# Optimization experiments

Hardware: AMD Instinct MI355X
Metric: run time of the kernel (lower is better)

## Reference

```python
import jax, jax.numpy as jnp
import numpy as np

B, T, SD = 16, 512, 64          # batch, action seq len, sample_dim
EMB, HD = 1024, 64              # emb_dim, head_dim
NH = EMB // HD                  # 16 heads
DEPTH, NREG, LAT, FF = 8, 16, 256, 4 * EMB
S = T + NREG                    # total sequence length (actions + registers)


def setup_inputs() -> dict:
    key = jax.random.key(0)
    ks = jax.random.split(key, 16)
    def n(k, shape, scale=0.02):
        return jax.random.normal(k, shape, jnp.float32) * scale
    return {
        "sample": jax.random.normal(ks[0], (B, T, SD), jnp.float32),
        "W_emb": n(ks[1], (SD, EMB)), "b_emb": jnp.zeros((EMB,), jnp.float32),
        "pos": n(ks[2], (T, EMB)),
        "registers": n(ks[3], (NREG, EMB), 1.0),
        "ln1_s": jnp.ones((DEPTH, EMB), jnp.float32), "ln1_b": jnp.zeros((DEPTH, EMB), jnp.float32),
        "W_qkv": n(ks[4], (DEPTH, EMB, 3 * EMB)), "b_qkv": jnp.zeros((DEPTH, 3 * EMB), jnp.float32),
        "W_o": n(ks[5], (DEPTH, EMB, EMB)), "b_o": jnp.zeros((DEPTH, EMB), jnp.float32),
        "ln2_s": jnp.ones((DEPTH, EMB), jnp.float32), "ln2_b": jnp.zeros((DEPTH, EMB), jnp.float32),
        "W_fc1": n(ks[6], (DEPTH, EMB, FF)), "b_fc1": jnp.zeros((DEPTH, FF), jnp.float32),
        "W_fc2": n(ks[7], (DEPTH, FF, EMB)), "b_fc2": jnp.zeros((DEPTH, EMB), jnp.float32),
        "lnf_s": jnp.ones((EMB,), jnp.float32), "lnf_b": jnp.zeros((EMB,), jnp.float32),
        "W_head": n(ks[8], (EMB, LAT)), "b_head": jnp.zeros((LAT,), jnp.float32),
    }


def _ln(x, s, b):
    m = jnp.mean(x, -1, keepdims=True)
    v = jnp.var(x, -1, keepdims=True)
    return (x - m) * jax.lax.rsqrt(v + 1e-5) * s + b


def _causal_last_mask():
    # True = attended to. Actions attend to all actions but NOT registers;
    # registers attend to all actions and causally (incl. self) to registers.
    allowed = jnp.ones((S, S), jnp.bool_)
    allowed = allowed.at[:T, T:].set(False)
    allowed = allowed.at[T:, T:].set(jnp.tril(jnp.ones((NREG, NREG), jnp.bool_)))
    return allowed


def reference(sample, W_emb, b_emb, pos, registers, ln1_s, ln1_b, W_qkv, b_qkv,
              W_o, b_o, ln2_s, ln2_b, W_fc1, b_fc1, W_fc2, b_fc2,
              lnf_s, lnf_b, W_head, b_head):
    # embed + positional add
    x = sample @ W_emb + b_emb + pos[None, :, :]          # [B,T,E]
    # concat registers
    x = jnp.concatenate([x, jnp.broadcast_to(registers, (B, NREG, EMB))], axis=1)  # [B,S,E]
    mask = _causal_last_mask()                             # [S,S]
    scale = 1.0 / jnp.sqrt(jnp.asarray(HD, x.dtype))
    for i in range(DEPTH):
        # pre-LN multi-head attention with structured block mask
        h = _ln(x, ln1_s[i], ln1_b[i])
        qkv = h @ W_qkv[i] + b_qkv[i]
        q, k, v = jnp.split(qkv, 3, axis=-1)
        q = q.reshape(B, S, NH, HD)
        k = k.reshape(B, S, NH, HD)
        v = v.reshape(B, S, NH, HD)
        att = jnp.einsum('bqhd,bkhd->bhqk', q, k) * scale
        att = jnp.where(mask[None, None], att, jnp.finfo(att.dtype).min)
        att = jax.nn.softmax(att, axis=-1)
        o = jnp.einsum('bhqk,bkhd->bqhd', att, v).reshape(B, S, EMB)
        x = x + o @ W_o[i] + b_o[i]
        # pre-LN MLP
        h2 = _ln(x, ln2_s[i], ln2_b[i])
        x = x + jax.nn.gelu(h2 @ W_fc1[i] + b_fc1[i]) @ W_fc2[i] + b_fc2[i]
    x = _ln(x, lnf_s, lnf_b)
    # head applied to register positions only
    return x[:, T:] @ W_head + b_head                      # [B,NREG,LAT]
```

## Files before the change

kernel.cpp:

```cpp
#include <hip/hip_runtime.h>
#include <hip/hip_bf16.h>


typedef unsigned short u16;
typedef __attribute__((ext_vector_type(4))) float f32x4;
typedef __attribute__((ext_vector_type(8))) __bf16 bf16x8;

#define DEV static __device__ __forceinline__

constexpr int Bb = 16, Tt = 512, E = 1024, HD = 64, NHd = 16;
constexpr int DEPTH = 8, NREG = 16, LAT = 256, FF = 4096;
constexpr int S = Tt + NREG;
constexpr int SPAD = 576;
constexpr int MR = Bb * S;
constexpr int ME = Bb * Tt;

DEV u16 f2bf(float f) {
  unsigned u = __builtin_bit_cast(unsigned, f);
  u += 0x7fffu + ((u >> 16) & 1u);
  return (u16)(u >> 16);
}

DEV void gll16(const u16* g, u16* l) {
  __builtin_amdgcn_global_load_lds((const __attribute__((address_space(1))) void*)g,
                                   (__attribute__((address_space(3))) void*)l, 16, 0, 0);
}

enum { M_EMBED, M_QKV, M_OPROJ, M_FC1, M_FC2, M_HEAD };

struct GA {
  const u16* A; const u16* Bt;
  int K, lda, ldb, Nrows, ldc;
  const float* bias; const float* pos;
  float* fout; u16* bout;
  u16 *qp, *kp, *vtp;
};

template<int MODE, int BN>
__global__ __launch_bounds__(256)
void gemm_bt(GA g) {
  constexpr int NI = BN / 32;
  __shared__ __align__(16) u16 As[128 * 32];
  __shared__ __align__(16) u16 Bs[BN * 32];
  const int tid = threadIdx.x;
  const u16* A  = g.A;
  const u16* Bt = g.Bt;
  const int tM = blockIdx.y, tN = blockIdx.x;

  const int lane = tid & 63, wid = tid >> 6;
  const int wr = wid >> 1, wc = wid & 1;
  const int fr = lane & 15, fg = lane >> 4;

  const int arow = tM * 128 + (tid >> 2);
  int br0 = tN * BN + (tid >> 2);
  if (br0 > g.Nrows - 1) br0 = g.Nrows - 1;
  int br1 = tN * BN + 64 + (tid >> 2);
  if (br1 > g.Nrows - 1) br1 = g.Nrows - 1;
  const int kseg = (tid & 3) * 8;
  u16* lA = As + (tid & 192) * 8;
  u16* lB = Bs + (tid & 192) * 8;

  f32x4 acc[4][NI];
#pragma unroll
  for (int i = 0; i < 4; ++i)
#pragma unroll
    for (int j = 0; j < NI; ++j) acc[i][j] = f32x4{0.f, 0.f, 0.f, 0.f};

  const int nk = g.K >> 5;
  for (int kt = 0; kt < nk; ++kt) {
    const int k0 = kt << 5;
    gll16(A + (long)arow        * g.lda + k0 + kseg, lA);
    gll16(A + (long)(arow + 64) * g.lda + k0 + kseg, lA + 2048);
    gll16(Bt + (long)br0        * g.ldb + k0 + kseg, lB);
    if (BN == 128)
      gll16(Bt + (long)br1      * g.ldb + k0 + kseg, lB + 2048);
    __syncthreads();
    bf16x8 af[4], bfr[NI];
#pragma unroll
    for (int mi = 0; mi < 4; ++mi)
      af[mi] = *(const bf16x8*)&As[(wr * 64 + mi * 16 + fr) * 32 + fg * 8];
#pragma unroll
    for (int ni = 0; ni < NI; ++ni)
      bfr[ni] = *(const bf16x8*)&Bs[(wc * (BN / 2) + ni * 16 + fr) * 32 + fg * 8];
#pragma unroll
    for (int mi = 0; mi < 4; ++mi)
#pragma unroll
      for (int ni = 0; ni < NI; ++ni)
        acc[mi][ni] = __builtin_amdgcn_mfma_f32_16x16x32_bf16(af[mi], bfr[ni], acc[mi][ni], 0, 0, 0);
    __syncthreads();
  }

#pragma unroll
  for (int mi = 0; mi < 4; ++mi)
#pragma unroll
    for (int ni = 0; ni < NI; ++ni)
#pragma unroll
      for (int j = 0; j < 4; ++j) {
        const int row = tM * 128 + wr * 64 + mi * 16 + fg * 4 + j;
        const int col = tN * BN + wc * (BN / 2) + ni * 16 + fr;
        float v = acc[mi][ni][j];
        if (MODE == M_EMBED) {
          const int b = row >> 9, t = row & 511;
          v += g.bias[col] + g.pos[(long)t * E + col];
          g.fout[((long)(b * S + t)) * E + col] = v;
        } else if (MODE == M_QKV) {
          const int b = row / S, s = row - b * S;
          v += g.bias[col];
          const int part = col >> 10, c = col & 1023;
          const int hh = c >> 6, d = c & 63;
          const u16 bf = f2bf(v);
          if (part == 0)      g.qp [((long)((b * NHd + hh) * SPAD + s)) * HD + d] = bf;
          else if (part == 1) g.kp [((long)((b * NHd + hh) * SPAD + s)) * HD + d] = bf;
          else                g.vtp[((long)((b * NHd + hh) * HD   + d)) * SPAD + s] = bf;
        } else if (MODE == M_OPROJ || MODE == M_FC2) {
          const long idx = (long)row * g.ldc + col;
          g.fout[idx] += v + g.bias[col];
        } else if (MODE == M_FC1) {
          v += g.bias[col];
          const float z = 0.7978845608028654f * (v + 0.044715f * v * v * v);
          const float e = __expf(2.f * z);
          const float th = 1.f - 2.f / (e + 1.f);
          g.bout[(long)row * g.ldc + col] = f2bf(0.5f * v * (1.f + th));
        } else if (MODE == M_HEAD) {
          g.fout[(long)row * g.ldc + col] = v + g.bias[col];
        }
      }
}

__global__ __launch_bounds__(256)
void flash_k(const u16* __restrict__ q, const u16* __restrict__ k,
             const u16* __restrict__ vt, u16* __restrict__ o) {
  __shared__ __align__(16) u16 Ks[64 * 64];
  __shared__ __align__(16) u16 Vs[64 * 64];
  __shared__ __align__(16) u16 Ps[4 * 16 * 64];
  const int tid = threadIdx.x;
  const int lane = tid & 63, w = tid >> 6;
  const int fr = lane & 15, fg = lane >> 4;
  const int qt = blockIdx.x, bh = blockIdx.y;
  const int q0 = qt * 64;

  const u16* qrow = q + ((long)bh * SPAD + q0 + w * 16 + fr) * HD;
  const bf16x8 qf0 = *(const bf16x8*)(qrow + fg * 8);
  const bf16x8 qf1 = *(const bf16x8*)(qrow + 32 + fg * 8);

  const int srow = lane >> 3, sseg = (lane & 7) * 8;
  const u16* kg = k  + ((long)bh * SPAD + w * 16 + srow) * HD + sseg;
  const u16* vg = vt + ((long)(bh * HD + w * 16 + srow)) * SPAD + sseg;
  u16* lk = Ks + w * 16 * HD;
  u16* lv = Vs + w * 16 * HD;

  float m[4], lsum[4]; f32x4 oa[4];
#pragma unroll
  for (int j = 0; j < 4; ++j) { m[j] = -1e30f; lsum[j] = 0.f; }
#pragma unroll
  for (int n = 0; n < 4; ++n) oa[n] = f32x4{0.f, 0.f, 0.f, 0.f};

  const int nt = (q0 < Tt) ? 8 : 9;
  for (int kt = 0; kt < nt; ++kt) {
    __syncthreads();
    gll16(kg + kt * 64 * HD,          lk);
    gll16(kg + kt * 64 * HD + 8 * HD, lk + 8 * HD);
    gll16(vg + kt * 64,               lv);
    gll16(vg + kt * 64 + 8 * SPAD,    lv + 8 * HD);
    __syncthreads();

    f32x4 sfr[4];
#pragma unroll
    for (int n = 0; n < 4; ++n) {
      const bf16x8 kf0 = *(const bf16x8*)&Ks[(n * 16 + fr) * HD + fg * 8];
      const bf16x8 kf1 = *(const bf16x8*)&Ks[(n * 16 + fr) * HD + 32 + fg * 8];
      sfr[n] = __builtin_amdgcn_mfma_f32_16x16x32_bf16(qf0, kf0, f32x4{0.f,0.f,0.f,0.f}, 0, 0, 0);
      sfr[n] = __builtin_amdgcn_mfma_f32_16x16x32_bf16(qf1, kf1, sfr[n], 0, 0, 0);
    }
    float p[4][4];
#pragma unroll
    for (int j = 0; j < 4; ++j) {
      const int qg = q0 + w * 16 + fg * 4 + j;
      const int vlim = qg < Tt ? Tt : qg + 1;
#pragma unroll
      for (int n = 0; n < 4; ++n) {
        const int col = kt * 64 + n * 16 + fr;
        p[n][j] = (col < vlim) ? sfr[n][j] * 0.125f : -1e30f;
      }
    }
#pragma unroll
    for (int j = 0; j < 4; ++j) {
      float pm = fmaxf(fmaxf(p[0][j], p[1][j]), fmaxf(p[2][j], p[3][j]));
#pragma unroll
      for (int msk = 1; msk <= 8; msk <<= 1) pm = fmaxf(pm, __shfl_xor(pm, msk));
      const float mn = fmaxf(m[j], pm);
      const float corr = __expf(m[j] - mn);
      m[j] = mn;
      float rs = 0.f;
#pragma unroll
      for (int n = 0; n < 4; ++n) { const float e = __expf(p[n][j] - mn); p[n][j] = e; rs += e; }
#pragma unroll
      for (int msk = 1; msk <= 8; msk <<= 1) rs += __shfl_xor(rs, msk);
      lsum[j] = lsum[j] * corr + rs;
#pragma unroll
      for (int n = 0; n < 4; ++n) oa[n][j] *= corr;
    }
#pragma unroll
    for (int j = 0; j < 4; ++j)
#pragma unroll
      for (int n = 0; n < 4; ++n)
        Ps[w * 1024 + (fg * 4 + j) * 64 + n * 16 + fr] = f2bf(p[n][j]);
    __syncthreads();
    const bf16x8 pf0 = *(const bf16x8*)&Ps[w * 1024 + fr * 64 + fg * 8];
    const bf16x8 pf1 = *(const bf16x8*)&Ps[w * 1024 + fr * 64 + 32 + fg * 8];
#pragma unroll
    for (int n = 0; n < 4; ++n) {
      const bf16x8 vf0 = *(const bf16x8*)&Vs[(n * 16 + fr) * HD + fg * 8];
      const bf16x8 vf1 = *(const bf16x8*)&Vs[(n * 16 + fr) * HD + 32 + fg * 8];
      oa[n] = __builtin_amdgcn_mfma_f32_16x16x32_bf16(pf0, vf0, oa[n], 0, 0, 0);
      oa[n] = __builtin_amdgcn_mfma_f32_16x16x32_bf16(pf1, vf1, oa[n], 0, 0, 0);
    }
  }

  const int b = bh >> 4, hh = bh & 15;
#pragma unroll
  for (int j = 0; j < 4; ++j) {
    const int qg = q0 + w * 16 + fg * 4 + j;
    if (qg < S) {
      const float inv = 1.f / lsum[j];
#pragma unroll
      for (int n = 0; n < 4; ++n)
        o[((long)(b * S + qg)) * E + hh * HD + n * 16 + fr] = f2bf(oa[n][j] * inv);
    }
  }
}

__global__ __launch_bounds__(256)
void ln_k(const float* __restrict__ x, const float* __restrict__ sc,
          const float* __restrict__ bi, u16* __restrict__ out, int gather) {
  const int r = blockIdx.x;
  const int srow = gather ? ((r >> 4) * S + Tt + (r & 15)) : r;
  const float4 v = ((const float4*)(x + (long)srow * E))[threadIdx.x];
  float s = v.x + v.y + v.z + v.w;
  float q = v.x * v.x + v.y * v.y + v.z * v.z + v.w * v.w;
#pragma unroll
  for (int o = 32; o; o >>= 1) { s += __shfl_down(s, o); q += __shfl_down(q, o); }
  __shared__ float ps[8];
  if ((threadIdx.x & 63) == 0) { ps[threadIdx.x >> 6] = s; ps[4 + (threadIdx.x >> 6)] = q; }
  __syncthreads();
  s = ps[0] + ps[1] + ps[2] + ps[3];
  q = ps[4] + ps[5] + ps[6] + ps[7];
  const float mean = s * (1.f / E);
  const float rs = rsqrtf(q * (1.f / E) - mean * mean + 1e-5f);
  const int c = threadIdx.x * 4;
  ushort4 o4;
  o4.x = f2bf((v.x - mean) * rs * sc[c + 0] + bi[c + 0]);
  o4.y = f2bf((v.y - mean) * rs * sc[c + 1] + bi[c + 1]);
  o4.z = f2bf((v.z - mean) * rs * sc[c + 2] + bi[c + 2]);
  o4.w = f2bf((v.w - mean) * rs * sc[c + 3] + bi[c + 3]);
  ((ushort4*)(out + (long)r * E))[threadIdx.x] = o4;
}

__global__ __launch_bounds__(256)
void wtrans(const float* __restrict__ src, u16* __restrict__ dst, int R, int C) {
  __shared__ float t[32][33];
  const int c0 = blockIdx.x * 32, r0 = blockIdx.y * 32;
  const int tx = threadIdx.x & 31, ty = threadIdx.x >> 5;
#pragma unroll
  for (int i = 0; i < 32; i += 8) t[ty + i][tx] = src[(long)(r0 + ty + i) * C + c0 + tx];
  __syncthreads();
#pragma unroll
  for (int i = 0; i < 32; i += 8) dst[(long)(c0 + ty + i) * R + r0 + tx] = f2bf(t[tx][ty + i]);
}

__global__ void cvt_bf(const float* __restrict__ in, u16* __restrict__ out, long n) {
  const long i = ((long)blockIdx.x * blockDim.x + threadIdx.x) * 4;
  if (i >= n) return;
  const float4 v = *(const float4*)(in + i);
  ushort4 o; o.x = f2bf(v.x); o.y = f2bf(v.y); o.z = f2bf(v.z); o.w = f2bf(v.w);
  *(ushort4*)(out + i) = o;
}

__global__ void zero_k(float4* p, long n) {
  long i = (long)blockIdx.x * blockDim.x + threadIdx.x;
  const long st = (long)gridDim.x * blockDim.x;
  const float4 z = make_float4(0.f, 0.f, 0.f, 0.f);
  for (; i < n; i += st) p[i] = z;
}

__global__ void reg_copy(const float* __restrict__ regs, float* __restrict__ x) {
  const int b = blockIdx.x >> 4, r = blockIdx.x & 15;
  const float4* sp = (const float4*)(regs + (long)r * E);
  float4* dp = (float4*)(x + ((long)(b * S + Tt + r)) * E);
  dp[threadIdx.x] = sp[threadIdx.x];
}

constexpr long OFF_WQKV = 0L;
constexpr long OFF_WO   = OFF_WQKV + 3072L * 1024 * 2;
constexpr long OFF_WFC1 = OFF_WO   + 1024L * 1024 * 2;
constexpr long OFF_WFC2 = OFF_WFC1 + 4096L * 1024 * 2;
constexpr long OFF_WEMB = OFF_WFC2 + 1024L * 4096 * 2;
constexpr long OFF_WHEAD= OFF_WEMB + 1024L * 64 * 2;
constexpr long OFF_SMP  = OFF_WHEAD+ 256L * 1024 * 2;
constexpr long OFF_X    = OFF_SMP  + (long)ME * 64 * 2;
constexpr long OFF_H    = OFF_X    + (long)MR * E * 4;
constexpr long OFF_Q    = OFF_H    + (long)MR * E * 2;
constexpr long OFF_K    = OFF_Q    + 256L * SPAD * HD * 2;
constexpr long OFF_VT   = OFF_K    + 256L * SPAD * HD * 2;
constexpr long OFF_O    = OFF_VT   + 256L * SPAD * HD * 2;
constexpr long OFF_HF   = OFF_O    + (long)MR * FF * 2;
constexpr long WS_NEED  = OFF_HF   + 256L * 1024 * 2;

extern "C" void kernel_launch(void* const* d_in, const int* in_sizes, int n_in,
                              void* d_out, int out_size, void* d_ws, size_t ws_size,
                              hipStream_t stream) {
  if (ws_size < (size_t)WS_NEED) return;

  const float* sample = (const float*)d_in[0];
  const float* W_emb  = (const float*)d_in[1];
  const float* b_emb  = (const float*)d_in[2];
  const float* pos    = (const float*)d_in[3];
  const float* regs   = (const float*)d_in[4];
  const float* ln1_s  = (const float*)d_in[5];
  const float* ln1_b  = (const float*)d_in[6];
  const float* W_qkv  = (const float*)d_in[7];
  const float* b_qkv  = (const float*)d_in[8];
  const float* W_o    = (const float*)d_in[9];
  const float* b_o    = (const float*)d_in[10];
  const float* ln2_s  = (const float*)d_in[11];
  const float* ln2_b  = (const float*)d_in[12];
  const float* W_fc1  = (const float*)d_in[13];
  const float* b_fc1  = (const float*)d_in[14];
  const float* W_fc2  = (const float*)d_in[15];
  const float* b_fc2  = (const float*)d_in[16];
  const float* lnf_s  = (const float*)d_in[17];
  const float* lnf_b  = (const float*)d_in[18];
  const float* W_head = (const float*)d_in[19];
  const float* b_head = (const float*)d_in[20];

  char* w = (char*)d_ws;
  u16* wqkvT = (u16*)(w + OFF_WQKV);
  u16* woT   = (u16*)(w + OFF_WO);
  u16* wfc1T = (u16*)(w + OFF_WFC1);
  u16* wfc2T = (u16*)(w + OFF_WFC2);
  u16* wembT = (u16*)(w + OFF_WEMB);
  u16* wheadT= (u16*)(w + OFF_WHEAD);
  u16* smp   = (u16*)(w + OFF_SMP);
  float* x   = (float*)(w + OFF_X);
  u16* h     = (u16*)(w + OFF_H);
  u16* qp    = (u16*)(w + OFF_Q);
  u16* kp    = (u16*)(w + OFF_K);
  u16* vtp   = (u16*)(w + OFF_VT);
  u16* o     = (u16*)(w + OFF_O);
  u16* a1    = (u16*)(w + OFF_O);
  u16* hf    = (u16*)(w + OFF_HF);

  wtrans<<<dim3(32, 2, 1), 256, 0, stream>>>(W_emb,  wembT, 64, 1024);
  wtrans<<<dim3(8, 32, 1), 256, 0, stream>>>(W_head, wheadT, 1024, 256);
  cvt_bf<<<dim3(512), 256, 0, stream>>>(sample, smp, (long)ME * 64);
  zero_k<<<dim3(2048), 256, 0, stream>>>((float4*)qp, (3L * 256 * SPAD * HD * 2) / 16);

  {
    GA g{}; g.A = smp; g.Bt = wembT; g.K = 64; g.lda = 64; g.ldb = 64;
    g.Nrows = E; g.bias = b_emb; g.pos = pos; g.fout = x;
    gemm_bt<M_EMBED, 64><<<dim3(16, 64, 1), 256, 0, stream>>>(g);
  }
  reg_copy<<<dim3(256), 256, 0, stream>>>(regs, x);

  for (int L = 0; L < DEPTH; ++L) {
    wtrans<<<dim3(96, 32, 1),  256, 0, stream>>>(W_qkv + (long)L * 1024 * 3072, wqkvT, 1024, 3072);
    wtrans<<<dim3(32, 32, 1),  256, 0, stream>>>(W_o   + (long)L * 1024 * 1024, woT,   1024, 1024);
    wtrans<<<dim3(128, 32, 1), 256, 0, stream>>>(W_fc1 + (long)L * 1024 * 4096, wfc1T, 1024, 4096);
    wtrans<<<dim3(32, 128, 1), 256, 0, stream>>>(W_fc2 + (long)L * 4096 * 1024, wfc2T, 4096, 1024);

    ln_k<<<dim3(MR), 256, 0, stream>>>(x, ln1_s + L * E, ln1_b + L * E, h, 0);
    {
      GA g{}; g.A = h; g.Bt = wqkvT;
      g.K = 1024; g.lda = 1024; g.ldb = 1024; g.Nrows = 3072;
      g.bias = b_qkv + L * 3072; g.qp = qp; g.kp = kp; g.vtp = vtp;
      gemm_bt<M_QKV, 128><<<dim3(24, 66, 1), 256, 0, stream>>>(g);
    }
    flash_k<<<dim3(9, 256, 1), 256, 0, stream>>>(qp, kp, vtp, o);
    {
      GA g{}; g.A = o; g.Bt = woT;
      g.K = 1024; g.lda = 1024; g.ldb = 1024; g.Nrows = 1024; g.ldc = 1024;
      g.bias = b_o + L * E; g.fout = x;
      gemm_bt<M_OPROJ, 64><<<dim3(16, 66, 1), 256, 0, stream>>>(g);
    }
    ln_k<<<dim3(MR), 256, 0, stream>>>(x, ln2_s + L * E, ln2_b + L * E, h, 0);
    {
      GA g{}; g.A = h; g.Bt = wfc1T;
      g.K = 1024; g.lda = 1024; g.ldb = 1024; g.Nrows = 4096; g.ldc = 4096;
      g.bias = b_fc1 + L * FF; g.bout = a1;
      gemm_bt<M_FC1, 128><<<dim3(32, 66, 1), 256, 0, stream>>>(g);
    }
    {
      GA g{}; g.A = a1; g.Bt = wfc2T;
      g.K = 4096; g.lda = 4096; g.ldb = 4096; g.Nrows = 1024; g.ldc = 1024;
      g.bias = b_fc2 + L * E; g.fout = x;
      gemm_bt<M_FC2, 64><<<dim3(16, 66, 1), 256, 0, stream>>>(g);
    }
  }

  ln_k<<<dim3(256), 256, 0, stream>>>(x, lnf_s, lnf_b, hf, 1);
  {
    GA g{}; g.A = hf; g.Bt = wheadT; g.K = 1024; g.lda = 1024; g.ldb = 1024;
    g.Nrows = LAT; g.ldc = LAT; g.bias = b_head; g.fout = (float*)d_out;
    gemm_bt<M_HEAD, 128><<<dim3(2, 2, 1), 256, 0, stream>>>(g);
  }
}
```

Baseline: 4.383 ms.

## Double-buffer GEMM LDS tiles, remap blocks across XCDs, widen O-proj/FC2 tiles

The GEMM kernel now keeps two LDS buffers and issues the global-to-LDS loads for the next K step before computing on the current one. This drops one barrier per iteration and lets memory traffic overlap the MFMA work. Workgroup indices in both the GEMM and flash-attention kernels are remapped so neighbouring tiles land on the same XCD, which is meant to improve L2 reuse. The O-projection and FC2 GEMMs switch from 64-wide to 128-wide N tiles, which halves their grid and doubles the LDS footprint. These changes could lower occupancy or wave-level parallelism.

```diff
diff --git a/kernel.cpp b/kernel.cpp
--- a/kernel.cpp
+++ b/kernel.cpp
@@ -40,12 +40,21 @@
 __global__ __launch_bounds__(256)
 void gemm_bt(GA g) {
   constexpr int NI = BN / 32;
-  __shared__ __align__(16) u16 As[128 * 32];
-  __shared__ __align__(16) u16 Bs[BN * 32];
+  __shared__ __align__(16) u16 As[2][128 * 32];
+  __shared__ __align__(16) u16 Bs[2][BN * 32];
   const int tid = threadIdx.x;
   const u16* A  = g.A;
   const u16* Bt = g.Bt;
-  const int tM = blockIdx.y, tN = blockIdx.x;
+
+  int tM, tN;
+  {
+    const int nwg = gridDim.x * gridDim.y;
+    int flat = blockIdx.y * gridDim.x + blockIdx.x;
+    const int q = nwg >> 3, r = nwg & 7;
+    const int xcd = flat & 7, loc = flat >> 3;
+    flat = (xcd < r ? xcd * (q + 1) : r * (q + 1) + (xcd - r) * q) + loc;
+    tM = flat / gridDim.x; tN = flat % gridDim.x;
+  }
 
   const int lane = tid & 63, wid = tid >> 6;
   const int wr = wid >> 1, wc = wid & 1;
@@ -57,8 +66,12 @@
   int br1 = tN * BN + 64 + (tid >> 2);
   if (br1 > g.Nrows - 1) br1 = g.Nrows - 1;
   const int kseg = (tid & 3) * 8;
-  u16* lA = As + (tid & 192) * 8;
-  u16* lB = Bs + (tid & 192) * 8;
+  const int woff = (tid & 192) * 8;
+
+  const u16* ag0 = A  + (long)arow        * g.lda + kseg;
+  const u16* ag1 = A  + (long)(arow + 64) * g.lda + kseg;
+  const u16* bg0 = Bt + (long)br0         * g.ldb + kseg;
+  const u16* bg1 = Bt + (long)br1         * g.ldb + kseg;
 
   f32x4 acc[4][NI];
 #pragma unroll
@@ -67,21 +80,30 @@
     for (int j = 0; j < NI; ++j) acc[i][j] = f32x4{0.f, 0.f, 0.f, 0.f};
 
   const int nk = g.K >> 5;
+  {
+    gll16(ag0, &As[0][woff]);
+    gll16(ag1, &As[0][woff + 2048]);
+    gll16(bg0, &Bs[0][woff]);
+    if (BN == 128) gll16(bg1, &Bs[0][woff + 2048]);
+  }
+  __syncthreads();
+
   for (int kt = 0; kt < nk; ++kt) {
-    const int k0 = kt << 5;
-    gll16(A + (long)arow        * g.lda + k0 + kseg, lA);
-    gll16(A + (long)(arow + 64) * g.lda + k0 + kseg, lA + 2048);
-    gll16(Bt + (long)br0        * g.ldb + k0 + kseg, lB);
-    if (BN == 128)
-      gll16(Bt + (long)br1      * g.ldb + k0 + kseg, lB + 2048);
-    __syncthreads();
+    const int cur = kt & 1;
+    if (kt + 1 < nk) {
+      const int k0 = (kt + 1) << 5;
+      gll16(ag0 + k0, &As[cur ^ 1][woff]);
+      gll16(ag1 + k0, &As[cur ^ 1][woff + 2048]);
+      gll16(bg0 + k0, &Bs[cur ^ 1][woff]);
+      if (BN == 128) gll16(bg1 + k0, &Bs[cur ^ 1][woff + 2048]);
+    }
     bf16x8 af[4], bfr[NI];
 #pragma unroll
     for (int mi = 0; mi < 4; ++mi)
-      af[mi] = *(const bf16x8*)&As[(wr * 64 + mi * 16 + fr) * 32 + fg * 8];
+      af[mi] = *(const bf16x8*)&As[cur][(wr * 64 + mi * 16 + fr) * 32 + fg * 8];
 #pragma unroll
     for (int ni = 0; ni < NI; ++ni)
-      bfr[ni] = *(const bf16x8*)&Bs[(wc * (BN / 2) + ni * 16 + fr) * 32 + fg * 8];
+      bfr[ni] = *(const bf16x8*)&Bs[cur][(wc * (BN / 2) + ni * 16 + fr) * 32 + fg * 8];
 #pragma unroll
     for (int mi = 0; mi < 4; ++mi)
 #pragma unroll
@@ -136,7 +158,10 @@
   const int tid = threadIdx.x;
   const int lane = tid & 63, w = tid >> 6;
   const int fr = lane & 15, fg = lane >> 4;
-  const int qt = blockIdx.x, bh = blockIdx.y;
+
+  int flat = blockIdx.y * 9 + blockIdx.x;
+  flat = (flat & 7) * 288 + (flat >> 3);
+  const int bh = flat / 9, qt = flat % 9;
   const int q0 = qt * 64;
 
   const u16* qrow = q + ((long)bh * SPAD + q0 + w * 16 + fr) * HD;
@@ -380,7 +405,7 @@
       GA g{}; g.A = o; g.Bt = woT;
       g.K = 1024; g.lda = 1024; g.ldb = 1024; g.Nrows = 1024; g.ldc = 1024;
       g.bias = b_o + L * E; g.fout = x;
-      gemm_bt<M_OPROJ, 64><<<dim3(16, 66, 1), 256, 0, stream>>>(g);
+      gemm_bt<M_OPROJ, 128><<<dim3(8, 66, 1), 256, 0, stream>>>(g);
     }
     ln_k<<<dim3(MR), 256, 0, stream>>>(x, ln2_s + L * E, ln2_b + L * E, h, 0);
     {
@@ -393,7 +418,7 @@
       GA g{}; g.A = a1; g.Bt = wfc2T;
       g.K = 4096; g.lda = 4096; g.ldb = 4096; g.Nrows = 1024; g.ldc = 1024;
       g.bias = b_fc2 + L * E; g.fout = x;
-      gemm_bt<M_FC2, 64><<<dim3(16, 66, 1), 256, 0, stream>>>(g);
+      gemm_bt<M_FC2, 128><<<dim3(8, 66, 1), 256, 0, stream>>>(g);
     }
   }
 
```

Measured after the change: 3.948 ms. 1.11x faster.
